# Kernel tuning notes

Measured on AMD Instinct MI355X. Metric: run time of the kernel, lower is better.

Reference implementation:

```python
import jax, jax.numpy as jnp
import numpy as np

B, N, C, H = 2, 2048, 512, 8
D = C // H  # head dim = 64
SCALE = C ** -0.5  # module uses heads_channels**-0.5 (full inner dim, not per-head)


def setup_inputs() -> dict:
    key = jax.random.key(0)
    ks = jax.random.split(key, 9)
    return {
        "q": jax.random.normal(ks[0], (B, N, C), jnp.float32),
        "kv": jax.random.normal(ks[1], (B, N, C), jnp.float32),
        "pos_q": jax.random.normal(ks[2], (B, N, D), jnp.float32),
        "pos_k": jax.random.normal(ks[3], (B, N, D), jnp.float32),
        "Wq": jax.random.normal(ks[4], (C, C), jnp.float32) * (C ** -0.5),
        "Wk": jax.random.normal(ks[5], (C, C), jnp.float32) * (C ** -0.5),
        "Wv": jax.random.normal(ks[6], (C, C), jnp.float32) * (C ** -0.5),
        "Wo": jax.random.normal(ks[7], (C, C), jnp.float32) * (C ** -0.5),
        "bo": jnp.zeros((C,), jnp.float32),
    }


def reference(q, kv, pos_q, pos_k, Wq, Wk, Wv, Wo, bo):
    # projections: [b n c] @ [c c] -> [b n c]
    qp = q @ Wq
    kp = kv @ Wk
    vp = kv @ Wv
    # split heads: b n (h d) -> b h n d
    split = lambda t: t.reshape(B, N, H, D).transpose(0, 2, 1, 3)
    qh, kh, vh = split(qp), split(kp), split(vp)
    # additive positional bias, broadcast over heads: b n d -> b 1 n d
    qh = qh + pos_q[:, None, :, :]
    kh = kh + pos_k[:, None, :, :]
    sim = jnp.einsum("bhid,bhjd->bhij", qh, kh) * SCALE
    attn = jax.nn.softmax(sim, axis=-1)
    out = jnp.einsum("bhij,bhjd->bhid", attn, vh)
    # merge heads: b h n d -> b n (h d)
    out = out.transpose(0, 2, 1, 3).reshape(B, N, C)
    return out @ Wo + bo
```

## Files before the change

kernel.cpp:

```cpp
#include <hip/hip_runtime.h>
#include <hip/hip_bf16.h>
#include <stdint.h>
#include <math.h>

static constexpr int kB = 2, kN = 2048, kC = 512, kH = 8, kD = 64;
static constexpr float kScaleL2E =
    (float)(0.044194173824159216 * 1.4426950408889634);
static constexpr float kShift = 12.0f;
static constexpr int kSplit = 4;
static constexpr size_t kSegF = (size_t)kB * kN * kC;

typedef short bf16x8 __attribute__((ext_vector_type(8)));
typedef short bf16x4 __attribute__((ext_vector_type(4)));
typedef float f32x4  __attribute__((ext_vector_type(4)));

__device__ __forceinline__ float bf2f(unsigned short u) {
  union { unsigned int i; float f; } v; v.i = ((unsigned int)u) << 16; return v.f;
}
__device__ __forceinline__ unsigned short f2bf(float f) {
  union { float f; unsigned int i; } v; v.f = f;
  unsigned int x = v.i;
  return (unsigned short)((x + 0x7FFFu + ((x >> 16) & 1u)) >> 16);
}
__device__ __forceinline__ short f2bs(float f) { return (short)f2bf(f); }
__device__ __forceinline__ unsigned int pack2_t(float lo, float hi) {
  union { float f; unsigned int i; } a, b; a.f = lo; b.f = hi;
  return (b.i & 0xFFFF0000u) | (a.i >> 16);
}

__device__ __forceinline__ f32x4 mfma16(bf16x4 a, bf16x4 b, f32x4 c) {
#if __has_builtin(__builtin_amdgcn_mfma_f32_16x16x16_bf16)
  return __builtin_amdgcn_mfma_f32_16x16x16_bf16(a, b, c, 0, 0, 0);
#else
  return __builtin_amdgcn_mfma_f32_16x16x16bf16_1k(a, b, c, 0, 0, 0);
#endif
}

__global__ __launch_bounds__(256) void prep_kernel(
    const float* __restrict__ q, const float* __restrict__ kv,
    const float* __restrict__ Wq, const float* __restrict__ Wk,
    const float* __restrict__ Wv,
    unsigned short* __restrict__ qbf, unsigned short* __restrict__ kvbf,
    unsigned short* __restrict__ wT)
{
  const int t = threadIdx.x;
  if (blockIdx.z == 0) {
    const int gid = blockIdx.x * 256 + t;
    #pragma unroll
    for (int it = 0; it < 8; ++it) {
      int i4 = gid + it * 65536;
      float4 a = *(const float4*)(q + (size_t)i4 * 4);
      float4 b = *(const float4*)(kv + (size_t)i4 * 4);
      bf16x4 ab = {f2bs(a.x), f2bs(a.y), f2bs(a.z), f2bs(a.w)};
      bf16x4 bb = {f2bs(b.x), f2bs(b.y), f2bs(b.z), f2bs(b.w)};
      *(bf16x4*)(qbf + (size_t)i4 * 4) = ab;
      *(bf16x4*)(kvbf + (size_t)i4 * 4) = bb;
    }
  } else {
    if (blockIdx.x >= 192) return;
    const int wsel = blockIdx.x >> 6;
    const int tile = blockIdx.x & 63;
    const int tr = tile >> 3, tc = tile & 7;
    const float* W = (wsel == 0) ? Wq : (wsel == 1 ? Wk : Wv);
    unsigned short* out = wT + (size_t)wsel * kC * kC;

    __shared__ __align__(16) float Ts[64][68];
    #pragma unroll
    for (int it = 0; it < 4; ++it) {
      int e = t + it * 256;
      int r = e >> 4, c4 = (e & 15) * 4;
      *(float4*)&Ts[r][c4] =
          *(const float4*)(W + (size_t)(tr * 64 + r) * kC + tc * 64 + c4);
    }
    __syncthreads();
    const int n = t >> 2, ks = (t & 3) * 16;
    unsigned short* orow = out + (size_t)(tc * 64 + n) * kC + tr * 64 + ks;
    #pragma unroll
    for (int c = 0; c < 4; ++c) {
      ushort4 o;
      o.x = f2bf(Ts[ks + c * 4 + 0][n]);
      o.y = f2bf(Ts[ks + c * 4 + 1][n]);
      o.z = f2bf(Ts[ks + c * 4 + 2][n]);
      o.w = f2bf(Ts[ks + c * 4 + 3][n]);
      *(ushort4*)(orow + c * 4) = o;
    }
  }
}

__global__ __launch_bounds__(256) void proj_kernel(
    const unsigned short* __restrict__ qbf,
    const unsigned short* __restrict__ kvbf,
    const unsigned short* __restrict__ wT,
    const float* __restrict__ pos_q,
    const float* __restrict__ pos_k,
    unsigned short* __restrict__ qh,
    unsigned short* __restrict__ kh,
    unsigned short* __restrict__ vhT)
{
  const bool kvmode = (blockIdx.z == 1);
  const unsigned short* A = kvmode ? kvbf : qbf;
  const unsigned short* Bt0 = wT + (kvmode ? (size_t)kC * kC : 0);
  const unsigned short* Bt1 = wT + 2 * (size_t)kC * kC;

  __shared__ __align__(16) unsigned short As[128][72];
  __shared__ __align__(16) unsigned short Bs[2][64][72];

  const int t = threadIdx.x;
  const int w = t >> 6, lane = t & 63;
  const int l15 = lane & 15, quad = lane >> 4;
  const int m0 = blockIdx.x * 128;
  const int n0 = blockIdx.y * 64;

  const int sr = t >> 3, sc = (t & 7) * 8;

  bf16x8 pa[4], pb0[2], pb1[2];
  #pragma unroll
  for (int i = 0; i < 4; ++i)
    pa[i] = *(const bf16x8*)(A + (size_t)(m0 + sr + i * 32) * kC + sc);
  #pragma unroll
  for (int i = 0; i < 2; ++i)
    pb0[i] = *(const bf16x8*)(Bt0 + (size_t)(n0 + sr + i * 32) * kC + sc);
  if (kvmode)
    #pragma unroll
    for (int i = 0; i < 2; ++i)
      pb1[i] = *(const bf16x8*)(Bt1 + (size_t)(n0 + sr + i * 32) * kC + sc);

  f32x4 acc0[2][4], acc1[2][4];
  #pragma unroll
  for (int si = 0; si < 2; ++si)
    #pragma unroll
    for (int ct = 0; ct < 4; ++ct) {
      acc0[si][ct] = (f32x4){0.f, 0.f, 0.f, 0.f};
      acc1[si][ct] = (f32x4){0.f, 0.f, 0.f, 0.f};
    }

  for (int k0 = 0; k0 < kC; k0 += 64) {
    if (k0) __syncthreads();
    #pragma unroll
    for (int i = 0; i < 4; ++i) *(bf16x8*)&As[sr + i * 32][sc] = pa[i];
    #pragma unroll
    for (int i = 0; i < 2; ++i) *(bf16x8*)&Bs[0][sr + i * 32][sc] = pb0[i];
    if (kvmode)
      #pragma unroll
      for (int i = 0; i < 2; ++i) *(bf16x8*)&Bs[1][sr + i * 32][sc] = pb1[i];
    __syncthreads();
    if (k0 + 64 < kC) {
      int kn = k0 + 64;
      #pragma unroll
      for (int i = 0; i < 4; ++i)
        pa[i] = *(const bf16x8*)(A + (size_t)(m0 + sr + i * 32) * kC + kn + sc);
      #pragma unroll
      for (int i = 0; i < 2; ++i)
        pb0[i] = *(const bf16x8*)(Bt0 + (size_t)(n0 + sr + i * 32) * kC + kn + sc);
      if (kvmode)
        #pragma unroll
        for (int i = 0; i < 2; ++i)
          pb1[i] = *(const bf16x8*)(Bt1 + (size_t)(n0 + sr + i * 32) * kC + kn + sc);
    }
    bf16x8 a0[2], a1[2];
    #pragma unroll
    for (int si = 0; si < 2; ++si) {
      a0[si] = *(const bf16x8*)&As[w * 32 + si * 16 + l15][quad * 8];
      a1[si] = *(const bf16x8*)&As[w * 32 + si * 16 + l15][32 + quad * 8];
    }
    #pragma unroll
    for (int ct = 0; ct < 4; ++ct) {
      bf16x8 b0 = *(const bf16x8*)&Bs[0][ct * 16 + l15][quad * 8];
      bf16x8 b1 = *(const bf16x8*)&Bs[0][ct * 16 + l15][32 + quad * 8];
      #pragma unroll
      for (int si = 0; si < 2; ++si) {
        acc0[si][ct] = __builtin_amdgcn_mfma_f32_16x16x32_bf16(a0[si], b0, acc0[si][ct], 0, 0, 0);
        acc0[si][ct] = __builtin_amdgcn_mfma_f32_16x16x32_bf16(a1[si], b1, acc0[si][ct], 0, 0, 0);
      }
      if (kvmode) {
        bf16x8 c0 = *(const bf16x8*)&Bs[1][ct * 16 + l15][quad * 8];
        bf16x8 c1 = *(const bf16x8*)&Bs[1][ct * 16 + l15][32 + quad * 8];
        #pragma unroll
        for (int si = 0; si < 2; ++si) {
          acc1[si][ct] = __builtin_amdgcn_mfma_f32_16x16x32_bf16(a0[si], c0, acc1[si][ct], 0, 0, 0);
          acc1[si][ct] = __builtin_amdgcn_mfma_f32_16x16x32_bf16(a1[si], c1, acc1[si][ct], 0, 0, 0);
        }
      }
    }
  }

  const int h = n0 >> 6;
  if (!kvmode) {
    #pragma unroll
    for (int si = 0; si < 2; ++si)
      #pragma unroll
      for (int r = 0; r < 4; ++r) {
        int m = m0 + w * 32 + si * 16 + quad * 4 + r;
        int b = m >> 11, n_seq = m & (kN - 1);
        #pragma unroll
        for (int ct = 0; ct < 4; ++ct) {
          int d = ct * 16 + l15;
          float val = (acc0[si][ct][r] +
                       pos_q[((size_t)b * kN + n_seq) * kD + d]) * kScaleL2E;
          qh[(((size_t)b * kH + h) * kN + n_seq) * kD + d] = f2bf(val);
        }
      }
  } else {
    #pragma unroll
    for (int si = 0; si < 2; ++si)
      #pragma unroll
      for (int r = 0; r < 4; ++r) {
        int m = m0 + w * 32 + si * 16 + quad * 4 + r;
        int b = m >> 11, n_seq = m & (kN - 1);
        #pragma unroll
        for (int ct = 0; ct < 4; ++ct) {
          int d = ct * 16 + l15;
          float vk = acc0[si][ct][r] + pos_k[((size_t)b * kN + n_seq) * kD + d];
          kh[(((size_t)b * kH + h) * kN + n_seq) * kD + d] = f2bf(vk);
        }
      }
    __syncthreads();
    unsigned short (*Tv)[136] = (unsigned short(*)[136])&As[0][0];
    #pragma unroll
    for (int si = 0; si < 2; ++si)
      #pragma unroll
      for (int ct = 0; ct < 4; ++ct) {
        const int d = ct * 16 + l15;
        const int nl = w * 32 + si * 16 + quad * 4;
        unsigned int lo = (unsigned int)f2bf(acc1[si][ct][0]) |
                          ((unsigned int)f2bf(acc1[si][ct][1]) << 16);
        unsigned int hi = (unsigned int)f2bf(acc1[si][ct][2]) |
                          ((unsigned int)f2bf(acc1[si][ct][3]) << 16);
        *(unsigned int*)&Tv[d][nl]     = lo;
        *(unsigned int*)&Tv[d][nl + 2] = hi;
      }
    __syncthreads();
    const int c16 = t & 15, dr = t >> 4;
    const int b2 = m0 >> 11, nbase = m0 & (kN - 1);
    #pragma unroll
    for (int rep = 0; rep < 4; ++rep) {
      const int d = rep * 16 + dr;
      bf16x8 vv = *(const bf16x8*)&Tv[d][c16 * 8];
      *(bf16x8*)(vhT + (((size_t)(b2 * kH + h)) * kD + d) * kN + nbase + c16 * 8) = vv;
    }
  }
}

__global__ __launch_bounds__(256, 4) void attn_kernel(
    const unsigned short* __restrict__ qh,
    const unsigned short* __restrict__ kh,
    const unsigned short* __restrict__ vhT,
    unsigned short* __restrict__ opart,
    float* __restrict__ lbuf)
{
  const int bh = blockIdx.y;
  const int b = bh >> 3, h = bh & 7;
  const int q0 = blockIdx.x * 128;
  const int s = blockIdx.z;
  const int kbase = s * (kN / kSplit);
  const int nkt = kN / kSplit / 64;
  const int t = threadIdx.x;
  const int w = t >> 6, lane = t & 63;
  const int l15 = lane & 15, quad = lane >> 4;

  __shared__ __align__(16) unsigned short Kbf[2][64][72];
  __shared__ __align__(16) unsigned short Vt[2][64][72];

  const unsigned short* Qb = qh  + (size_t)bh * kN * kD;
  const unsigned short* Kb = kh  + (size_t)bh * kN * kD;
  const unsigned short* Vb = vhT + (size_t)bh * kD * kN;

  bf16x8 aq[2][2];
  #pragma unroll
  for (int g = 0; g < 2; ++g) {
    const unsigned short* qrow = Qb + (size_t)(q0 + w * 32 + g * 16 + l15) * kD;
    aq[g][0] = *(const bf16x8*)(qrow + quad * 8);
    aq[g][1] = *(const bf16x8*)(qrow + 32 + quad * 8);
  }

  const int sr = t >> 3, sc = (t & 7) * 8, sr2 = sr + 32;
  const int vc0 = ((sc >> 2) & 3) * 16 + (sc >> 4) * 4;

  bf16x8 pk0 = *(const bf16x8*)(Kb + (size_t)(kbase + sr) * kD + sc);
  bf16x8 pk1 = *(const bf16x8*)(Kb + (size_t)(kbase + sr2) * kD + sc);
  bf16x8 pv0 = *(const bf16x8*)(Vb + (size_t)sr * kN + kbase + sc);
  bf16x8 pv1 = *(const bf16x8*)(Vb + (size_t)sr2 * kN + kbase + sc);
  *(bf16x8*)&Kbf[0][sr][sc]  = pk0;
  *(bf16x8*)&Kbf[0][sr2][sc] = pk1;
  {
    bf16x4 lo0 = {pv0[0], pv0[1], pv0[2], pv0[3]};
    bf16x4 hi0 = {pv0[4], pv0[5], pv0[6], pv0[7]};
    bf16x4 lo1 = {pv1[0], pv1[1], pv1[2], pv1[3]};
    bf16x4 hi1 = {pv1[4], pv1[5], pv1[6], pv1[7]};
    *(bf16x4*)&Vt[0][sr][vc0]       = lo0;
    *(bf16x4*)&Vt[0][sr][vc0 + 16]  = hi0;
    *(bf16x4*)&Vt[0][sr2][vc0]      = lo1;
    *(bf16x4*)&Vt[0][sr2][vc0 + 16] = hi1;
  }
  {
    int kt1 = kbase + 64;
    pk0 = *(const bf16x8*)(Kb + (size_t)(kt1 + sr) * kD + sc);
    pk1 = *(const bf16x8*)(Kb + (size_t)(kt1 + sr2) * kD + sc);
    pv0 = *(const bf16x8*)(Vb + (size_t)sr * kN + kt1 + sc);
    pv1 = *(const bf16x8*)(Vb + (size_t)sr2 * kN + kt1 + sc);
  }

  f32x4 o[2][4];
  #pragma unroll
  for (int g = 0; g < 2; ++g)
    #pragma unroll
    for (int nt = 0; nt < 4; ++nt) o[g][nt] = (f32x4){0.f, 0.f, 0.f, 0.f};
  float l_run[2] = {0.f, 0.f};

  for (int i = 0; i < nkt; ++i) {
    __syncthreads();
    if (i + 1 < nkt) {
      unsigned short (*Kw)[72] = Kbf[(i + 1) & 1];
      unsigned short (*Vw)[72] = Vt[(i + 1) & 1];
      *(bf16x8*)&Kw[sr][sc]  = pk0;
      *(bf16x8*)&Kw[sr2][sc] = pk1;
      bf16x4 lo0 = {pv0[0], pv0[1], pv0[2], pv0[3]};
      bf16x4 hi0 = {pv0[4], pv0[5], pv0[6], pv0[7]};
      bf16x4 lo1 = {pv1[0], pv1[1], pv1[2], pv1[3]};
      bf16x4 hi1 = {pv1[4], pv1[5], pv1[6], pv1[7]};
      *(bf16x4*)&Vw[sr][vc0]       = lo0;
      *(bf16x4*)&Vw[sr][vc0 + 16]  = hi0;
      *(bf16x4*)&Vw[sr2][vc0]      = lo1;
      *(bf16x4*)&Vw[sr2][vc0 + 16] = hi1;
      if (i + 2 < nkt) {
        int ktn = kbase + (i + 2) * 64;
        pk0 = *(const bf16x8*)(Kb + (size_t)(ktn + sr) * kD + sc);
        pk1 = *(const bf16x8*)(Kb + (size_t)(ktn + sr2) * kD + sc);
        pv0 = *(const bf16x8*)(Vb + (size_t)sr * kN + ktn + sc);
        pv1 = *(const bf16x8*)(Vb + (size_t)sr2 * kN + ktn + sc);
      }
    }
    const unsigned short (*Kr)[72] = Kbf[i & 1];
    const unsigned short (*Vr)[72] = Vt[i & 1];

    f32x4 sacc[2][4];
    __builtin_amdgcn_s_setprio(1);
    #pragma unroll
    for (int ct = 0; ct < 4; ++ct) {
      bf16x8 ak0 = *(const bf16x8*)&Kr[ct * 16 + l15][quad * 8];
      bf16x8 ak1 = *(const bf16x8*)&Kr[ct * 16 + l15][32 + quad * 8];
      #pragma unroll
      for (int g = 0; g < 2; ++g) {
        f32x4 zz = (f32x4){0.f, 0.f, 0.f, 0.f};
        zz = __builtin_amdgcn_mfma_f32_16x16x32_bf16(ak0, aq[g][0], zz, 0, 0, 0);
        zz = __builtin_amdgcn_mfma_f32_16x16x32_bf16(ak1, aq[g][1], zz, 0, 0, 0);
        sacc[g][ct] = zz;
      }
    }
    __builtin_amdgcn_s_setprio(0);

    union PB { unsigned int u[2]; bf16x4 v; } pb[2][4];
    #pragma unroll
    for (int g = 0; g < 2; ++g) {
      float psum = 0.f;
      #pragma unroll
      for (int ct = 0; ct < 4; ++ct)
        #pragma unroll
        for (int r = 0; r < 4; ++r) {
          float p = exp2f(sacc[g][ct][r] - kShift);
          sacc[g][ct][r] = p;
          psum += p;
        }
      psum += __shfl_xor(psum, 16);
      psum += __shfl_xor(psum, 32);
      l_run[g] += psum;
      #pragma unroll
      for (int ct = 0; ct < 4; ++ct) {
        pb[g][ct].u[0] = pack2_t(sacc[g][ct][0], sacc[g][ct][1]);
        pb[g][ct].u[1] = pack2_t(sacc[g][ct][2], sacc[g][ct][3]);
      }
    }

    __builtin_amdgcn_s_setprio(1);
    #pragma unroll
    for (int nt = 0; nt < 4; ++nt) {
      bf16x8 av0 = *(const bf16x8*)&Vr[nt * 16 + l15][quad * 16];
      bf16x8 av1 = *(const bf16x8*)&Vr[nt * 16 + l15][quad * 16 + 8];
      bf16x4 a_ct0 = {av0[0], av0[1], av0[2], av0[3]};
      bf16x4 a_ct1 = {av0[4], av0[5], av0[6], av0[7]};
      bf16x4 a_ct2 = {av1[0], av1[1], av1[2], av1[3]};
      bf16x4 a_ct3 = {av1[4], av1[5], av1[6], av1[7]};
      #pragma unroll
      for (int g = 0; g < 2; ++g) {
        o[g][nt] = mfma16(a_ct0, pb[g][0].v, o[g][nt]);
        o[g][nt] = mfma16(a_ct1, pb[g][1].v, o[g][nt]);
        o[g][nt] = mfma16(a_ct2, pb[g][2].v, o[g][nt]);
        o[g][nt] = mfma16(a_ct3, pb[g][3].v, o[g][nt]);
      }
    }
    __builtin_amdgcn_s_setprio(0);
  }

  if (quad == 0)
    #pragma unroll
    for (int g = 0; g < 2; ++g)
      lbuf[(size_t)(s * 16 + bh) * kN + q0 + w * 32 + g * 16 + l15] = l_run[g];

  __syncthreads();
  unsigned short (*Ot)[72] = (unsigned short(*)[72])&Kbf[0][0][0];
  #pragma unroll
  for (int g = 0; g < 2; ++g) {
    const int ql = w * 32 + g * 16 + l15;
    #pragma unroll
    for (int nt = 0; nt < 4; ++nt) {
      unsigned int lo = (unsigned int)f2bf(o[g][nt][0]) |
                        ((unsigned int)f2bf(o[g][nt][1]) << 16);
      unsigned int hi = (unsigned int)f2bf(o[g][nt][2]) |
                        ((unsigned int)f2bf(o[g][nt][3]) << 16);
      const int d0 = nt * 16 + quad * 4;
      *(unsigned int*)&Ot[ql][d0]     = lo;
      *(unsigned int*)&Ot[ql][d0 + 2] = hi;
    }
  }
  __syncthreads();
  {
    unsigned short* od = opart + (size_t)s * kSegF;
    const int c8 = t & 7, qb = t >> 3;
    #pragma unroll
    for (int rep = 0; rep < 4; ++rep) {
      const int ql = rep * 32 + qb;
      bf16x8 vv = *(const bf16x8*)&Ot[ql][c8 * 8];
      *(bf16x8*)(od + ((size_t)b * kN + (q0 + ql)) * kC + h * kD + c8 * 8) = vv;
    }
  }
}

__global__ __launch_bounds__(256) void proj_out_kernel(
    const unsigned short* __restrict__ opart,
    const float* __restrict__ lbuf,
    const float* __restrict__ Wo,
    const float* __restrict__ bo,
    float* __restrict__ out)
{
  __shared__ __align__(16) unsigned short Wt[64][72];

  const int t = threadIdx.x;
  const int w = t >> 6, lane = t & 63;
  const int l15 = lane & 15, quad = lane >> 4;
  const int m0 = blockIdx.x * 64;
  const int n0 = blockIdx.y * 64;

  const int m = m0 + w * 16 + l15;
  const int nseq = m & (kN - 1);
  const int bb = m >> 11;
  const size_t arow = (size_t)m * kC;

  ushort4 pw[4];
  #pragma unroll
  for (int i = 0; i < 4; ++i) {
    int e = t + i * 256;
    int r = e >> 4, c4 = (e & 15) * 4;
    float4 wv = *(const float4*)(Wo + (size_t)r * kC + n0 + c4);
    pw[i] = make_ushort4(f2bf(wv.x), f2bf(wv.y), f2bf(wv.z), f2bf(wv.w));
  }

  f32x4 acc[4];
  #pragma unroll
  for (int ct = 0; ct < 4; ++ct) acc[ct] = (f32x4){0.f, 0.f, 0.f, 0.f};

  #pragma unroll
  for (int k0 = 0; k0 < kC; k0 += 64) {
    if (k0) __syncthreads();
    #pragma unroll
    for (int i = 0; i < 4; ++i) {
      int e = t + i * 256;
      int r = e >> 4, c4 = (e & 15) * 4;
      Wt[c4 + 0][r] = pw[i].x;
      Wt[c4 + 1][r] = pw[i].y;
      Wt[c4 + 2][r] = pw[i].z;
      Wt[c4 + 3][r] = pw[i].w;
    }
    __syncthreads();

    const int h = k0 >> 6;
    const int bh = bb * 8 + h;
    float lsum = 0.f;
    #pragma unroll
    for (int s = 0; s < kSplit; ++s)
      lsum += lbuf[(size_t)(s * 16 + bh) * kN + nseq];
    const float wgt = 1.f / lsum;

    float af0[8] = {}, af1[8] = {};
    #pragma unroll
    for (int s = 0; s < kSplit; ++s) {
      bf16x8 v0 = *(const bf16x8*)(opart + (size_t)s * kSegF + arow + k0 + quad * 8);
      bf16x8 v1 = *(const bf16x8*)(opart + (size_t)s * kSegF + arow + k0 + 32 + quad * 8);
      #pragma unroll
      for (int j = 0; j < 8; ++j) {
        af0[j] += bf2f((unsigned short)v0[j]);
        af1[j] += bf2f((unsigned short)v1[j]);
      }
    }
    bf16x8 a0, a1;
    #pragma unroll
    for (int j = 0; j < 8; ++j) {
      a0[j] = (short)f2bf(af0[j] * wgt);
      a1[j] = (short)f2bf(af1[j] * wgt);
    }

    if (k0 + 64 < kC) {
      int kn = k0 + 64;
      #pragma unroll
      for (int i = 0; i < 4; ++i) {
        int e = t + i * 256;
        int r = e >> 4, c4 = (e & 15) * 4;
        float4 wv = *(const float4*)(Wo + (size_t)(kn + r) * kC + n0 + c4);
        pw[i] = make_ushort4(f2bf(wv.x), f2bf(wv.y), f2bf(wv.z), f2bf(wv.w));
      }
    }
    #pragma unroll
    for (int ct = 0; ct < 4; ++ct) {
      bf16x8 b0 = *(const bf16x8*)&Wt[ct * 16 + l15][quad * 8];
      bf16x8 b1 = *(const bf16x8*)&Wt[ct * 16 + l15][32 + quad * 8];
      acc[ct] = __builtin_amdgcn_mfma_f32_16x16x32_bf16(a0, b0, acc[ct], 0, 0, 0);
      acc[ct] = __builtin_amdgcn_mfma_f32_16x16x32_bf16(a1, b1, acc[ct], 0, 0, 0);
    }
  }

  #pragma unroll
  for (int ct = 0; ct < 4; ++ct) {
    int n = n0 + ct * 16 + l15;
    float bb2 = bo[n];
    #pragma unroll
    for (int r = 0; r < 4; ++r) {
      int mm = m0 + w * 16 + quad * 4 + r;
      out[(size_t)mm * kC + n] = acc[ct][r] + bb2;
    }
  }
}

extern "C" void kernel_launch(void* const* d_in, const int* in_sizes, int n_in,
                              void* d_out, int out_size, void* d_ws, size_t ws_size,
                              hipStream_t stream) {
  (void)in_sizes; (void)n_in; (void)out_size; (void)ws_size;
  const float* q     = (const float*)d_in[0];
  const float* kv    = (const float*)d_in[1];
  const float* pos_q = (const float*)d_in[2];
  const float* pos_k = (const float*)d_in[3];
  const float* Wq    = (const float*)d_in[4];
  const float* Wk    = (const float*)d_in[5];
  const float* Wv    = (const float*)d_in[6];
  const float* Wo    = (const float*)d_in[7];
  const float* bo    = (const float*)d_in[8];
  float* out = (float*)d_out;

  const size_t seg = (size_t)kB * kH * kN * kD;

  unsigned short* qbf  = (unsigned short*)d_ws;
  unsigned short* kvbf = qbf + seg;
  unsigned short* wT   = kvbf + seg;
  unsigned short* qhp  = wT + 3 * (size_t)kC * kC;
  unsigned short* khp  = qhp + seg;
  unsigned short* vtp  = khp + seg;
  unsigned short* opart = vtp + seg;
  float* lbuf = (float*)(opart + (size_t)kSplit * kSegF);

  dim3 blk(256);
  prep_kernel<<<dim3(256, 1, 2), blk, 0, stream>>>(q, kv, Wq, Wk, Wv, qbf, kvbf, wT);
  proj_kernel<<<dim3(32, 8, 2), blk, 0, stream>>>(qbf, kvbf, wT, pos_q, pos_k,
                                                  qhp, khp, vtp);
  attn_kernel<<<dim3(16, 16, kSplit), blk, 0, stream>>>(qhp, khp, vtp, opart, lbuf);
  proj_out_kernel<<<dim3(64, 8), blk, 0, stream>>>(opart, lbuf, Wo, bo, out);
}
```

Before: 158.9 us.

## Use 16x16x32 MFMA for PV product with remapped V smem layout

Replaces the four 16x16x16 bf16 MFMAs per output tile in the P@V step with two 16x16x32 MFMAs. To match, the V tile's shared-memory column permutation is changed so each lane's K fragment comes out as a contiguous 8-element load, and the P fragments are packed into bf16x8 registers. It also defers the cross-lane row-sum shuffles from every tile iteration to a single reduction after the loop. This cuts MFMA issue count and per-iteration shuffle work, at the risk of a layout mismatch between the new V permutation and the x32 MFMA's K ordering.

```diff
diff --git a/kernel.cpp b/kernel.cpp
--- a/kernel.cpp
+++ b/kernel.cpp
@@ -28,12 +28,8 @@
   return (b.i & 0xFFFF0000u) | (a.i >> 16);
 }
 
-__device__ __forceinline__ f32x4 mfma16(bf16x4 a, bf16x4 b, f32x4 c) {
-#if __has_builtin(__builtin_amdgcn_mfma_f32_16x16x16_bf16)
-  return __builtin_amdgcn_mfma_f32_16x16x16_bf16(a, b, c, 0, 0, 0);
-#else
-  return __builtin_amdgcn_mfma_f32_16x16x16bf16_1k(a, b, c, 0, 0, 0);
-#endif
+__device__ __forceinline__ int vcol(int k) {
+  return 32 * (k >> 5) + ((k >> 2) & 3) * 8 + ((k >> 4) & 1) * 4;
 }
 
 __global__ __launch_bounds__(256) void prep_kernel(
@@ -274,7 +270,7 @@
   }
 
   const int sr = t >> 3, sc = (t & 7) * 8, sr2 = sr + 32;
-  const int vc0 = ((sc >> 2) & 3) * 16 + (sc >> 4) * 4;
+  const int vc1 = vcol(sc), vc2 = vcol(sc + 4);
 
   bf16x8 pk0 = *(const bf16x8*)(Kb + (size_t)(kbase + sr) * kD + sc);
   bf16x8 pk1 = *(const bf16x8*)(Kb + (size_t)(kbase + sr2) * kD + sc);
@@ -287,10 +283,10 @@
     bf16x4 hi0 = {pv0[4], pv0[5], pv0[6], pv0[7]};
     bf16x4 lo1 = {pv1[0], pv1[1], pv1[2], pv1[3]};
     bf16x4 hi1 = {pv1[4], pv1[5], pv1[6], pv1[7]};
-    *(bf16x4*)&Vt[0][sr][vc0]       = lo0;
-    *(bf16x4*)&Vt[0][sr][vc0 + 16]  = hi0;
-    *(bf16x4*)&Vt[0][sr2][vc0]      = lo1;
-    *(bf16x4*)&Vt[0][sr2][vc0 + 16] = hi1;
+    *(bf16x4*)&Vt[0][sr][vc1]  = lo0;
+    *(bf16x4*)&Vt[0][sr][vc2]  = hi0;
+    *(bf16x4*)&Vt[0][sr2][vc1] = lo1;
+    *(bf16x4*)&Vt[0][sr2][vc2] = hi1;
   }
   {
     int kt1 = kbase + 64;
@@ -318,10 +314,10 @@
       bf16x4 hi0 = {pv0[4], pv0[5], pv0[6], pv0[7]};
       bf16x4 lo1 = {pv1[0], pv1[1], pv1[2], pv1[3]};
       bf16x4 hi1 = {pv1[4], pv1[5], pv1[6], pv1[7]};
-      *(bf16x4*)&Vw[sr][vc0]       = lo0;
-      *(bf16x4*)&Vw[sr][vc0 + 16]  = hi0;
-      *(bf16x4*)&Vw[sr2][vc0]      = lo1;
-      *(bf16x4*)&Vw[sr2][vc0 + 16] = hi1;
+      *(bf16x4*)&Vw[sr][vc1]  = lo0;
+      *(bf16x4*)&Vw[sr][vc2]  = hi0;
+      *(bf16x4*)&Vw[sr2][vc1] = lo1;
+      *(bf16x4*)&Vw[sr2][vc2] = hi1;
       if (i + 2 < nkt) {
         int ktn = kbase + (i + 2) * 64;
         pk0 = *(const bf16x8*)(Kb + (size_t)(ktn + sr) * kD + sc);
@@ -349,7 +345,7 @@
     }
     __builtin_amdgcn_s_setprio(0);
 
-    union PB { unsigned int u[2]; bf16x4 v; } pb[2][4];
+    union PB8 { unsigned int u[4]; bf16x8 v; } pb01[2], pb23[2];
     #pragma unroll
     for (int g = 0; g < 2; ++g) {
       float psum = 0.f;
@@ -361,36 +357,36 @@
           sacc[g][ct][r] = p;
           psum += p;
         }
-      psum += __shfl_xor(psum, 16);
-      psum += __shfl_xor(psum, 32);
       l_run[g] += psum;
-      #pragma unroll
-      for (int ct = 0; ct < 4; ++ct) {
-        pb[g][ct].u[0] = pack2_t(sacc[g][ct][0], sacc[g][ct][1]);
-        pb[g][ct].u[1] = pack2_t(sacc[g][ct][2], sacc[g][ct][3]);
-      }
+      pb01[g].u[0] = pack2_t(sacc[g][0][0], sacc[g][0][1]);
+      pb01[g].u[1] = pack2_t(sacc[g][0][2], sacc[g][0][3]);
+      pb01[g].u[2] = pack2_t(sacc[g][1][0], sacc[g][1][1]);
+      pb01[g].u[3] = pack2_t(sacc[g][1][2], sacc[g][1][3]);
+      pb23[g].u[0] = pack2_t(sacc[g][2][0], sacc[g][2][1]);
+      pb23[g].u[1] = pack2_t(sacc[g][2][2], sacc[g][2][3]);
+      pb23[g].u[2] = pack2_t(sacc[g][3][0], sacc[g][3][1]);
+      pb23[g].u[3] = pack2_t(sacc[g][3][2], sacc[g][3][3]);
     }
 
     __builtin_amdgcn_s_setprio(1);
     #pragma unroll
     for (int nt = 0; nt < 4; ++nt) {
-      bf16x8 av0 = *(const bf16x8*)&Vr[nt * 16 + l15][quad * 16];
-      bf16x8 av1 = *(const bf16x8*)&Vr[nt * 16 + l15][quad * 16 + 8];
-      bf16x4 a_ct0 = {av0[0], av0[1], av0[2], av0[3]};
-      bf16x4 a_ct1 = {av0[4], av0[5], av0[6], av0[7]};
-      bf16x4 a_ct2 = {av1[0], av1[1], av1[2], av1[3]};
-      bf16x4 a_ct3 = {av1[4], av1[5], av1[6], av1[7]};
+      bf16x8 av0 = *(const bf16x8*)&Vr[nt * 16 + l15][quad * 8];
+      bf16x8 av1 = *(const bf16x8*)&Vr[nt * 16 + l15][32 + quad * 8];
       #pragma unroll
       for (int g = 0; g < 2; ++g) {
-        o[g][nt] = mfma16(a_ct0, pb[g][0].v, o[g][nt]);
-        o[g][nt] = mfma16(a_ct1, pb[g][1].v, o[g][nt]);
-        o[g][nt] = mfma16(a_ct2, pb[g][2].v, o[g][nt]);
-        o[g][nt] = mfma16(a_ct3, pb[g][3].v, o[g][nt]);
+        o[g][nt] = __builtin_amdgcn_mfma_f32_16x16x32_bf16(av0, pb01[g].v, o[g][nt], 0, 0, 0);
+        o[g][nt] = __builtin_amdgcn_mfma_f32_16x16x32_bf16(av1, pb23[g].v, o[g][nt], 0, 0, 0);
       }
     }
     __builtin_amdgcn_s_setprio(0);
   }
 
+  #pragma unroll
+  for (int g = 0; g < 2; ++g) {
+    l_run[g] += __shfl_xor(l_run[g], 16);
+    l_run[g] += __shfl_xor(l_run[g], 32);
+  }
   if (quad == 0)
     #pragma unroll
     for (int g = 0; g < 2; ++g)
```

Result: no change. 161.6 us (+1.7%).
